# Kernel tuning notes

Hardware: AMD Instinct MI355X
Metric: run time of the kernel (lower is better)

## Reference

```python
import jax, jax.numpy as jnp
import numpy as np

EPS = 1e-8
TEMP = 0.05

def setup_inputs() -> dict:
    key = jax.random.key(0)
    ks = jax.random.split(key, 7)
    B, S, IN, OUT, R, K = 4, 4096, 4096, 4096, 8, 4
    x = jax.random.normal(ks[0], (B, S, IN), dtype=jnp.float32)
    V_shared = jax.random.normal(ks[1], (R, IN), dtype=jnp.float32) * 0.01
    U_shared = jax.random.normal(ks[2], (OUT, R), dtype=jnp.float32) * 0.01
    core_pool = jax.random.normal(ks[3], (K, R, R), dtype=jnp.float32)
    core_keys = jax.random.normal(ks[4], (K, IN), dtype=jnp.float32)
    gate_w = jax.random.normal(ks[5], (1, 2 * R), dtype=jnp.float32) * 0.1
    gate_b = jnp.ones((1,), dtype=jnp.float32)
    return {"x": x, "V_shared": V_shared, "U_shared": U_shared,
            "core_pool": core_pool, "core_keys": core_keys,
            "gate_w": gate_w, "gate_b": gate_b}

def reference(x, V_shared, U_shared, core_pool, core_keys, gate_w, gate_b):
    # --- Hebbian cosine router (eval mode: keys are fixed buffers) ---
    centroid = 0.7 * x[:, -1, :] + 0.3 * jnp.mean(x, axis=1)          # [B, in]
    cn = centroid / jnp.maximum(jnp.linalg.norm(centroid, axis=-1, keepdims=True), EPS)
    kn = core_keys / jnp.maximum(jnp.linalg.norm(core_keys, axis=-1, keepdims=True), EPS)
    sim = cn @ kn.T                                                     # [B, K]
    route_weights = jax.nn.softmax(sim / TEMP, axis=-1)                 # [B, K]
    # --- Soft core mixture: per-batch rank x rank matrix ---
    Lam_active = jnp.einsum('bk,kij->bij', route_weights, core_pool)    # [B, r, r]
    # --- Low-rank chain: x @ V^T @ Lam^T @ U^T ---
    x_V = jnp.einsum('bsi,ri->bsr', x, V_shared)                        # [B, S, r]
    x_V_Lam = jnp.einsum('bsr,bjr->bsj', x_V, Lam_active)               # bmm with Lam^T
    adapt_out = jnp.einsum('bsj,oj->bso', x_V_Lam, U_shared)            # [B, S, out]
    # --- GainLoRA sigmoid gate (scalar), gate input detached ---
    gate_in = jax.lax.stop_gradient(
        jnp.concatenate([U_shared.mean(axis=0), V_shared.mean(axis=1)], axis=0))  # [2r]
    gate = jax.nn.sigmoid(gate_w @ gate_in + gate_b)                    # [1]
    return gate[0] * adapt_out
```

## Files before the change

kernel.cpp:

```cpp
#include <hip/hip_runtime.h>
#include <math.h>

#define B_   4
#define S_   4096
#define IN_  4096
#define OUT_ 4096
#define RNK  8
#define K_   4

#define HALFC 2048
#define NKCH  8

typedef float f4v __attribute__((ext_vector_type(4)));

__global__ __launch_bounds__(256) void zK(float* __restrict__ p) {
    p[blockIdx.x * 256 + threadIdx.x] = 0.f;
}

__global__ __launch_bounds__(512, 4) void kA(const float* __restrict__ x,
                                             const float* __restrict__ V,
                                             float* __restrict__ colsum,
                                             float* __restrict__ xvp)
{
    __shared__ float Vsh[RNK][HALFC];
    __shared__ float shcs[4][512];
    const int tid = threadIdx.x;

    const int blk  = blockIdx.x;
    const int b    = blk >> 8;
    const int rem  = blk & 255;
    const int sblk = rem >> 1;
    const int half = rem & 1;
    const int c0   = half * HALFC;

    for (int i = tid; i < 2048; i += 512) ((float*)shcs)[i] = 0.f;

    for (int i = tid; i < (RNK * HALFC / 4); i += 512) {
        const int r  = i >> 9;
        const int cc = (i & 511) * 4;
        *(float4*)&Vsh[r][cc] = *(const float4*)(V + (size_t)r * IN_ + c0 + cc);
    }
    __syncthreads();

    const int w = tid >> 6, l = tid & 63;
    const int s0 = sblk * 32 + w * 4;
    const float* xb = x + ((size_t)(b * S_ + s0)) * IN_ + c0 + l * 4;

    float acc[4][8];
    #pragma unroll
    for (int row = 0; row < 4; ++row)
        #pragma unroll
        for (int r = 0; r < 8; ++r) acc[row][r] = 0.f;

    #pragma unroll 2
    for (int k = 0; k < NKCH; ++k) {
        const int col = k * 256 + l * 4;
        float4 xr[4];
        #pragma unroll
        for (int row = 0; row < 4; ++row)
            xr[row] = *(const float4*)(xb + (size_t)row * IN_ + k * 256);
        float4 vr[8];
        #pragma unroll
        for (int r = 0; r < 8; ++r) vr[r] = *(const float4*)&Vsh[r][col];

        #pragma unroll
        for (int row = 0; row < 4; ++row) {
            #pragma unroll
            for (int r = 0; r < 8; ++r)
                acc[row][r] += xr[row].x * vr[r].x + xr[row].y * vr[r].y
                             + xr[row].z * vr[r].z + xr[row].w * vr[r].w;
        }

        const float c0s = xr[0].x + xr[1].x + xr[2].x + xr[3].x;
        const float c1s = xr[0].y + xr[1].y + xr[2].y + xr[3].y;
        const float c2s = xr[0].z + xr[1].z + xr[2].z + xr[3].z;
        const float c3s = xr[0].w + xr[1].w + xr[2].w + xr[3].w;
        const int q = k * 64 + l;
        atomicAdd(&shcs[0][q], c0s);
        atomicAdd(&shcs[1][q], c1s);
        atomicAdd(&shcs[2][q], c2s);
        atomicAdd(&shcs[3][q], c3s);
    }

    #pragma unroll
    for (int m = 1; m <= 32; m <<= 1)
        #pragma unroll
        for (int row = 0; row < 4; ++row)
            #pragma unroll
            for (int r = 0; r < 8; ++r)
                acc[row][r] += __shfl_xor(acc[row][r], m);

    if (l == 0) {
        float* xo = xvp + (size_t)half * (B_ * S_ * RNK)
                        + ((size_t)(b * S_ + s0)) * RNK;
        #pragma unroll
        for (int row = 0; row < 4; ++row) {
            *(float4*)(xo + row * RNK)     = make_float4(acc[row][0], acc[row][1],
                                                         acc[row][2], acc[row][3]);
            *(float4*)(xo + row * RNK + 4) = make_float4(acc[row][4], acc[row][5],
                                                         acc[row][6], acc[row][7]);
        }
    }

    __syncthreads();
    for (int i = tid; i < 2048; i += 512) {
        const int comp = i >> 9, q = i & 511;
        unsafeAtomicAdd(&colsum[(size_t)b * IN_ + c0 + q * 4 + comp], ((float*)shcs)[i]);
    }
}

__global__ __launch_bounds__(1024) void kB(const float* __restrict__ x,
                                           const float* __restrict__ V,
                                           const float* __restrict__ U,
                                           const float* __restrict__ core_pool,
                                           const float* __restrict__ core_keys,
                                           const float* __restrict__ gate_w,
                                           const float* __restrict__ gate_b,
                                           const float* __restrict__ colsum,
                                           float* __restrict__ P)
{
    const int b = blockIdx.x, tid = threadIdx.x;
    float nrm2 = 0.f;
    float dotk[K_] = {0.f,0.f,0.f,0.f};
    float kn2[K_]  = {0.f,0.f,0.f,0.f};
    float us[8] = {0.f,0.f,0.f,0.f,0.f,0.f,0.f,0.f};
    float vs[8] = {0.f,0.f,0.f,0.f,0.f,0.f,0.f,0.f};

    const float ms = 0.3f / (float)S_;
    {
        const int c = tid * 4;
        const float4 cs = *(const float4*)(colsum + (size_t)b * IN_ + c);
        const float4 xl = *(const float4*)(x + ((size_t)(b * S_ + S_ - 1)) * IN_ + c);
        float4 cen;
        cen.x = 0.7f * xl.x + ms * cs.x;
        cen.y = 0.7f * xl.y + ms * cs.y;
        cen.z = 0.7f * xl.z + ms * cs.z;
        cen.w = 0.7f * xl.w + ms * cs.w;
        nrm2 += cen.x*cen.x + cen.y*cen.y + cen.z*cen.z + cen.w*cen.w;
        #pragma unroll
        for (int k = 0; k < K_; ++k) {
            const float4 ck = *(const float4*)(core_keys + (size_t)k * IN_ + c);
            dotk[k] += cen.x*ck.x + cen.y*ck.y + cen.z*ck.z + cen.w*ck.w;
            kn2[k]  += ck.x*ck.x + ck.y*ck.y + ck.z*ck.z + ck.w*ck.w;
        }
    }
    for (int o = tid; o < OUT_; o += 1024) {
        const float4 a  = *(const float4*)(U + (size_t)o * RNK);
        const float4 b4 = *(const float4*)(U + (size_t)o * RNK + 4);
        us[0]+=a.x;  us[1]+=a.y;  us[2]+=a.z;  us[3]+=a.w;
        us[4]+=b4.x; us[5]+=b4.y; us[6]+=b4.z; us[7]+=b4.w;
    }
    {
        const int c = tid * 4;
        #pragma unroll
        for (int r = 0; r < 8; ++r) {
            const float4 v = *(const float4*)(V + (size_t)r * IN_ + c);
            vs[r] += v.x + v.y + v.z + v.w;
        }
    }

    __shared__ float red[25 * 16];
    __shared__ float res[25];
    float vals[25];
    vals[0] = nrm2;
    #pragma unroll
    for (int k = 0; k < K_; ++k) { vals[1 + k] = dotk[k]; vals[5 + k] = kn2[k]; }
    #pragma unroll
    for (int r = 0; r < 8; ++r) { vals[9 + r] = us[r]; vals[17 + r] = vs[r]; }
    const int wid = tid >> 6, lane = tid & 63;
    #pragma unroll
    for (int i = 0; i < 25; ++i) {
        float v = vals[i];
        #pragma unroll
        for (int m = 32; m >= 1; m >>= 1) v += __shfl_xor(v, m);
        if (lane == 0) red[i * 16 + wid] = v;
    }
    __syncthreads();
    if (tid < 25) {
        float t = 0.f;
        #pragma unroll
        for (int j = 0; j < 16; ++j) t += red[tid * 16 + j];
        res[tid] = t;
    }
    __syncthreads();

    const float ncen = fmaxf(sqrtf(res[0]), 1e-8f);
    float lg[K_], mx = -1e30f;
    #pragma unroll
    for (int k = 0; k < K_; ++k) {
        const float nk = fmaxf(sqrtf(res[5 + k]), 1e-8f);
        lg[k] = (res[1 + k] / (ncen * nk)) * 20.0f;
        mx = fmaxf(mx, lg[k]);
    }
    float wk[K_], se = 0.f;
    #pragma unroll
    for (int k = 0; k < K_; ++k) { wk[k] = expf(lg[k] - mx); se += wk[k]; }
    const float inv_se = 1.f / se;
    float z = gate_b[0];
    #pragma unroll
    for (int r = 0; r < 8; ++r) z += gate_w[r]     * (res[9 + r]  * (1.f / OUT_));
    #pragma unroll
    for (int r = 0; r < 8; ++r) z += gate_w[8 + r] * (res[17 + r] * (1.f / IN_));
    const float gate = 1.f / (1.f + expf(-z));

    __shared__ float Tsh[64];
    if (tid < 64) {
        float acc = 0.f;
        #pragma unroll
        for (int k = 0; k < K_; ++k) acc += (wk[k] * inv_se) * core_pool[k * 64 + tid];
        Tsh[tid] = gate * acc;
    }
    __syncthreads();

    for (int o = tid; o < OUT_; o += 1024) {
        const float4 a  = *(const float4*)(U + (size_t)o * RNK);
        const float4 b4 = *(const float4*)(U + (size_t)o * RNK + 4);
        const float u[8] = {a.x, a.y, a.z, a.w, b4.x, b4.y, b4.z, b4.w};
        float pr[8];
        #pragma unroll
        for (int r = 0; r < 8; ++r) {
            float acc = 0.f;
            #pragma unroll
            for (int jj = 0; jj < 8; ++jj) acc += u[jj] * Tsh[jj * 8 + r];
            pr[r] = acc;
        }
        *(float4*)(P + (size_t)(b * OUT_ + o) * RNK)     = make_float4(pr[0], pr[1], pr[2], pr[3]);
        *(float4*)(P + (size_t)(b * OUT_ + o) * RNK + 4) = make_float4(pr[4], pr[5], pr[6], pr[7]);
    }
}

__global__ __launch_bounds__(256) void kD(const float* __restrict__ P,
                                          const float* __restrict__ xv,
                                          float* __restrict__ out)
{
    const int blk = blockIdx.x;
    const int b = blk >> 9, rem = blk & 511;
    const int half = rem >> 8, sc = rem & 255;
    const int t = threadIdx.x;
    const int oA = half * 2048 + t * 4;

    float PA[4][8], PB[4][8];
    #pragma unroll
    for (int u = 0; u < 4; ++u) {
        const float* pp = P + ((size_t)(b * OUT_ + oA + u)) * RNK;
        const float4 a = *(const float4*)pp;
        const float4 c = *(const float4*)(pp + 4);
        PA[u][0]=a.x; PA[u][1]=a.y; PA[u][2]=a.z; PA[u][3]=a.w;
        PA[u][4]=c.x; PA[u][5]=c.y; PA[u][6]=c.z; PA[u][7]=c.w;
        const float* pq = pp + (size_t)1024 * RNK;
        const float4 d = *(const float4*)pq;
        const float4 e = *(const float4*)(pq + 4);
        PB[u][0]=d.x; PB[u][1]=d.y; PB[u][2]=d.z; PB[u][3]=d.w;
        PB[u][4]=e.x; PB[u][5]=e.y; PB[u][6]=e.z; PB[u][7]=e.w;
    }

    const int srow0 = sc * 16;
    const float* xq0 = xv + ((size_t)(b * S_ + srow0)) * RNK;
    const float* xq1 = xq0 + (size_t)(B_ * S_ * RNK);
    float* op = out + ((size_t)(b * S_ + srow0)) * OUT_ + oA;
    #pragma unroll 4
    for (int row = 0; row < 16; ++row) {
        const float4 xa = *(const float4*)(xq0 + row * RNK);
        const float4 xb = *(const float4*)(xq0 + row * RNK + 4);
        const float4 ya = *(const float4*)(xq1 + row * RNK);
        const float4 yb = *(const float4*)(xq1 + row * RNK + 4);
        const float xr[8] = {xa.x+ya.x, xa.y+ya.y, xa.z+ya.z, xa.w+ya.w,
                             xb.x+yb.x, xb.y+yb.y, xb.z+yb.z, xb.w+yb.w};
        float accA[4], accB[4];
        #pragma unroll
        for (int u = 0; u < 4; ++u) {
            float sA = 0.f, sB = 0.f;
            #pragma unroll
            for (int r = 0; r < 8; ++r) { sA += PA[u][r] * xr[r]; sB += PB[u][r] * xr[r]; }
            accA[u] = sA; accB[u] = sB;
        }
        f4v vA = {accA[0], accA[1], accA[2], accA[3]};
        f4v vB = {accB[0], accB[1], accB[2], accB[3]};
        __builtin_nontemporal_store(vA, (f4v*)(op + (size_t)row * OUT_));
        __builtin_nontemporal_store(vB, (f4v*)(op + (size_t)row * OUT_ + 1024));
    }
}

extern "C" void kernel_launch(void* const* d_in, const int* in_sizes, int n_in,
                              void* d_out, int out_size, void* d_ws, size_t ws_size,
                              hipStream_t stream) {
    const float* x         = (const float*)d_in[0];
    const float* V         = (const float*)d_in[1];
    const float* U         = (const float*)d_in[2];
    const float* core_pool = (const float*)d_in[3];
    const float* core_keys = (const float*)d_in[4];
    const float* gate_w    = (const float*)d_in[5];
    const float* gate_b    = (const float*)d_in[6];
    float* out = (float*)d_out;

    float* colsum = (float*)d_ws;
    float* xv = colsum + (size_t)B_ * IN_;
    float* P  = xv + (size_t)2 * B_ * S_ * RNK;

    zK<<<dim3((B_ * IN_) / 256), dim3(256), 0, stream>>>(colsum);
    kA<<<dim3(1024), dim3(512), 0, stream>>>(x, V, colsum, xv);
    kB<<<dim3(B_), dim3(1024), 0, stream>>>(x, V, U, core_pool, core_keys,
                                            gate_w, gate_b, colsum, P);
    kD<<<dim3(2048), dim3(256), 0, stream>>>(P, xv, out);
}
```

Before: 495.9 us.

## Fold U-times-core projection into output kernel and prefetch x in kA

```diff
diff --git a/kernel.cpp b/kernel.cpp
--- a/kernel.cpp
+++ b/kernel.cpp
@@ -52,13 +52,19 @@
         #pragma unroll
         for (int r = 0; r < 8; ++r) acc[row][r] = 0.f;
 
-    #pragma unroll 2
+    float4 xr[4];
+    #pragma unroll
+    for (int row = 0; row < 4; ++row)
+        xr[row] = *(const float4*)(xb + (size_t)row * IN_);
+
     for (int k = 0; k < NKCH; ++k) {
+        float4 xn[4];
+        if (k < NKCH - 1) {
+            #pragma unroll
+            for (int row = 0; row < 4; ++row)
+                xn[row] = *(const float4*)(xb + (size_t)row * IN_ + (k + 1) * 256);
+        }
         const int col = k * 256 + l * 4;
-        float4 xr[4];
-        #pragma unroll
-        for (int row = 0; row < 4; ++row)
-            xr[row] = *(const float4*)(xb + (size_t)row * IN_ + k * 256);
         float4 vr[8];
         #pragma unroll
         for (int r = 0; r < 8; ++r) vr[r] = *(const float4*)&Vsh[r][col];
@@ -80,6 +86,11 @@
         atomicAdd(&shcs[1][q], c1s);
         atomicAdd(&shcs[2][q], c2s);
         atomicAdd(&shcs[3][q], c3s);
+
+        if (k < NKCH - 1) {
+            #pragma unroll
+            for (int row = 0; row < 4; ++row) xr[row] = xn[row];
+        }
     }
 
     #pragma unroll
@@ -109,7 +120,7 @@
     }
 }
 
-__global__ __launch_bounds__(1024) void kB(const float* __restrict__ x,
+__global__ __launch_bounds__(1024) void kR(const float* __restrict__ x,
                                            const float* __restrict__ V,
                                            const float* __restrict__ U,
                                            const float* __restrict__ core_pool,
@@ -117,7 +128,7 @@
                                            const float* __restrict__ gate_w,
                                            const float* __restrict__ gate_b,
                                            const float* __restrict__ colsum,
-                                           float* __restrict__ P)
+                                           float* __restrict__ gT)
 {
     const int b = blockIdx.x, tid = threadIdx.x;
     float nrm2 = 0.f;
@@ -184,52 +195,35 @@
     }
     __syncthreads();
 
-    const float ncen = fmaxf(sqrtf(res[0]), 1e-8f);
-    float lg[K_], mx = -1e30f;
-    #pragma unroll
-    for (int k = 0; k < K_; ++k) {
-        const float nk = fmaxf(sqrtf(res[5 + k]), 1e-8f);
-        lg[k] = (res[1 + k] / (ncen * nk)) * 20.0f;
-        mx = fmaxf(mx, lg[k]);
-    }
-    float wk[K_], se = 0.f;
-    #pragma unroll
-    for (int k = 0; k < K_; ++k) { wk[k] = expf(lg[k] - mx); se += wk[k]; }
-    const float inv_se = 1.f / se;
-    float z = gate_b[0];
-    #pragma unroll
-    for (int r = 0; r < 8; ++r) z += gate_w[r]     * (res[9 + r]  * (1.f / OUT_));
-    #pragma unroll
-    for (int r = 0; r < 8; ++r) z += gate_w[8 + r] * (res[17 + r] * (1.f / IN_));
-    const float gate = 1.f / (1.f + expf(-z));
-
-    __shared__ float Tsh[64];
     if (tid < 64) {
+        const float ncen = fmaxf(sqrtf(res[0]), 1e-8f);
+        float lg[K_], mx = -1e30f;
+        #pragma unroll
+        for (int k = 0; k < K_; ++k) {
+            const float nk = fmaxf(sqrtf(res[5 + k]), 1e-8f);
+            lg[k] = (res[1 + k] / (ncen * nk)) * 20.0f;
+            mx = fmaxf(mx, lg[k]);
+        }
+        float wk[K_], se = 0.f;
+        #pragma unroll
+        for (int k = 0; k < K_; ++k) { wk[k] = expf(lg[k] - mx); se += wk[k]; }
+        const float inv_se = 1.f / se;
+        float z = gate_b[0];
+        #pragma unroll
+        for (int r = 0; r < 8; ++r) z += gate_w[r]     * (res[9 + r]  * (1.f / OUT_));
+        #pragma unroll
+        for (int r = 0; r < 8; ++r) z += gate_w[8 + r] * (res[17 + r] * (1.f / IN_));
+        const float gate = 1.f / (1.f + expf(-z));
+
         float acc = 0.f;
         #pragma unroll
         for (int k = 0; k < K_; ++k) acc += (wk[k] * inv_se) * core_pool[k * 64 + tid];
-        Tsh[tid] = gate * acc;
-    }
-    __syncthreads();
-
-    for (int o = tid; o < OUT_; o += 1024) {
-        const float4 a  = *(const float4*)(U + (size_t)o * RNK);
-        const float4 b4 = *(const float4*)(U + (size_t)o * RNK + 4);
-        const float u[8] = {a.x, a.y, a.z, a.w, b4.x, b4.y, b4.z, b4.w};
-        float pr[8];
-        #pragma unroll
-        for (int r = 0; r < 8; ++r) {
-            float acc = 0.f;
-            #pragma unroll
-            for (int jj = 0; jj < 8; ++jj) acc += u[jj] * Tsh[jj * 8 + r];
-            pr[r] = acc;
-        }
-        *(float4*)(P + (size_t)(b * OUT_ + o) * RNK)     = make_float4(pr[0], pr[1], pr[2], pr[3]);
-        *(float4*)(P + (size_t)(b * OUT_ + o) * RNK + 4) = make_float4(pr[4], pr[5], pr[6], pr[7]);
-    }
-}
-
-__global__ __launch_bounds__(256) void kD(const float* __restrict__ P,
+        gT[b * 64 + tid] = gate * acc;
+    }
+}
+
+__global__ __launch_bounds__(256) void kD(const float* __restrict__ U,
+                                          const float* __restrict__ gT,
                                           const float* __restrict__ xv,
                                           float* __restrict__ out)
 {
@@ -239,19 +233,31 @@
     const int t = threadIdx.x;
     const int oA = half * 2048 + t * 4;
 
+    __shared__ float Tsh[64];
+    if (t < 64) Tsh[t] = gT[b * 64 + t];
+    __syncthreads();
+
     float PA[4][8], PB[4][8];
     #pragma unroll
     for (int u = 0; u < 4; ++u) {
-        const float* pp = P + ((size_t)(b * OUT_ + oA + u)) * RNK;
-        const float4 a = *(const float4*)pp;
-        const float4 c = *(const float4*)(pp + 4);
-        PA[u][0]=a.x; PA[u][1]=a.y; PA[u][2]=a.z; PA[u][3]=a.w;
-        PA[u][4]=c.x; PA[u][5]=c.y; PA[u][6]=c.z; PA[u][7]=c.w;
-        const float* pq = pp + (size_t)1024 * RNK;
-        const float4 d = *(const float4*)pq;
-        const float4 e = *(const float4*)(pq + 4);
-        PB[u][0]=d.x; PB[u][1]=d.y; PB[u][2]=d.z; PB[u][3]=d.w;
-        PB[u][4]=e.x; PB[u][5]=e.y; PB[u][6]=e.z; PB[u][7]=e.w;
+        const float* up = U + (size_t)(oA + u) * RNK;
+        const float4 a = *(const float4*)up;
+        const float4 c = *(const float4*)(up + 4);
+        const float ua[8] = {a.x, a.y, a.z, a.w, c.x, c.y, c.z, c.w};
+        const float* uq = up + (size_t)1024 * RNK;
+        const float4 d = *(const float4*)uq;
+        const float4 e = *(const float4*)(uq + 4);
+        const float ub[8] = {d.x, d.y, d.z, d.w, e.x, e.y, e.z, e.w};
+        #pragma unroll
+        for (int r = 0; r < 8; ++r) {
+            float sA = 0.f, sB = 0.f;
+            #pragma unroll
+            for (int jj = 0; jj < 8; ++jj) {
+                sA += ua[jj] * Tsh[jj * 8 + r];
+                sB += ub[jj] * Tsh[jj * 8 + r];
+            }
+            PA[u][r] = sA; PB[u][r] = sB;
+        }
     }
 
     const int srow0 = sc * 16;
@@ -295,11 +301,11 @@
 
     float* colsum = (float*)d_ws;
     float* xv = colsum + (size_t)B_ * IN_;
-    float* P  = xv + (size_t)2 * B_ * S_ * RNK;
+    float* gT = xv + (size_t)2 * B_ * S_ * RNK;
 
     zK<<<dim3((B_ * IN_) / 256), dim3(256), 0, stream>>>(colsum);
     kA<<<dim3(1024), dim3(512), 0, stream>>>(x, V, colsum, xv);
-    kB<<<dim3(B_), dim3(1024), 0, stream>>>(x, V, U, core_pool, core_keys,
-                                            gate_w, gate_b, colsum, P);
-    kD<<<dim3(2048), dim3(256), 0, stream>>>(P, xv, out);
-}
+    kR<<<dim3(B_), dim3(1024), 0, stream>>>(x, V, U, core_pool, core_keys,
+                                            gate_w, gate_b, colsum, gT);
+    kD<<<dim3(2048), dim3(256), 0, stream>>>(U, gT, xv, out);
+}
```

Result: no change. 495.7 us (-0.1%).
